# Kernel tuning notes

Hardware: AMD Instinct MI355X
Metric: run time of the kernel (lower is better)

## Reference

```python
import jax, jax.numpy as jnp
import numpy as np

B, S, D, H = 2, 2048, 2048, 16
HD = D // H  # 128
ROPE_BASE = 10000.0


def _rope_tables(seq_len, head_dim, dtype=jnp.float32):
    inv_freq = 1.0 / (ROPE_BASE ** (jnp.arange(0, head_dim, 2, dtype=jnp.float32) / head_dim))
    t = jnp.arange(seq_len, dtype=jnp.float32)
    freqs = jnp.outer(t, inv_freq)  # [S, HD/2]
    # broadcast shape [1, S, 1, HD/2]
    return jnp.cos(freqs)[None, :, None, :].astype(dtype), jnp.sin(freqs)[None, :, None, :].astype(dtype)


def _apply_rope(x, cos, sin):
    # x: [B, S, H, HD]; interleaved split, output concatenated by halves (matches torch code)
    x1 = x[..., ::2]
    x2 = x[..., 1::2]
    return jnp.concatenate([x1 * cos - x2 * sin, x1 * sin + x2 * cos], axis=-1)


def setup_inputs() -> dict:
    key = jax.random.key(0)
    ks = jax.random.split(key, 9)
    xavier = lambda k: jax.random.uniform(k, (D, D), jnp.float32, -1.0, 1.0) * np.sqrt(6.0 / (D + D))
    return {
        "x": jax.random.normal(ks[0], (B, S, D), jnp.float32),
        "attention_mask": jnp.ones((B, S), jnp.int32),
        "wq": xavier(ks[1]), "bq": jnp.zeros((D,), jnp.float32),
        "wk": xavier(ks[2]), "bk": jnp.zeros((D,), jnp.float32),
        "wv": xavier(ks[3]), "bv": jnp.zeros((D,), jnp.float32),
        "wo": xavier(ks[4]), "bo": jnp.zeros((D,), jnp.float32),
    }


def reference(x, attention_mask, wq, bq, wk, bk, wv, bv, wo, bo):
    b, s, _ = x.shape
    scale = HD ** -0.5
    q = (x @ wq + bq).reshape(b, s, H, HD)
    k = (x @ wk + bk).reshape(b, s, H, HD)
    v = (x @ wv + bv).reshape(b, s, H, HD)
    cos, sin = _rope_tables(s, HD, x.dtype)
    q = _apply_rope(q, cos, sin)
    k = _apply_rope(k, cos, sin)
    # [B, H, S, S]
    scores = jnp.einsum('bqhd,bkhd->bhqk', q, k) * scale
    mask = attention_mask[:, None, None, :]  # 2D mask -> [B,1,1,S]
    scores = jnp.where(mask == 0, jnp.asarray(-1e9, scores.dtype), scores)
    attn = jax.nn.softmax(scores, axis=-1)
    out = jnp.einsum('bhqk,bkhd->bqhd', attn, v).reshape(b, s, D)
    return out @ wo + bo
```

## Files before the change

### kernel.cpp

```cpp
#include <hip/hip_runtime.h>

#define Bc 2
#define Sc 2048
#define Dc 2048
#define Hc 16
#define HDc 128
#define Mc 4096

typedef __bf16 bf16_t;
typedef __bf16 bf16x4 __attribute__((ext_vector_type(4)));
typedef __bf16 bf16x8 __attribute__((ext_vector_type(8)));
typedef float f32x4 __attribute__((ext_vector_type(4)));
typedef float f32x16 __attribute__((ext_vector_type(16)));

__device__ __forceinline__ f32x4 mfma16(bf16x8 a, bf16x8 b, f32x4 c) {
  return __builtin_amdgcn_mfma_f32_16x16x32_bf16(a, b, c, 0, 0, 0);
}
__device__ __forceinline__ f32x16 mfma32(bf16x8 a, bf16x8 b, f32x16 c) {
  return __builtin_amdgcn_mfma_f32_32x32x16_bf16(a, b, c, 0, 0, 0);
}

typedef const unsigned __attribute__((address_space(1))) gu32_t;
typedef unsigned __attribute__((address_space(3))) lu32_t;

__device__ __forceinline__ void gload_lds16(const void* g, void* l) {
  gu32_t* gp = (gu32_t*)(unsigned long long)g;
  lu32_t* lp = (lu32_t*)(unsigned)(unsigned long long)l;
  __builtin_amdgcn_global_load_lds(gp, lp, 16, 0, 0);
}

__device__ __forceinline__ unsigned cvtpk(float lo, float hi_) {
  unsigned r;
  asm("v_cvt_pk_bf16_f32 %0, %1, %2" : "=v"(r) : "v"(lo), "v"(hi_));
  return r;
}
__device__ __forceinline__ void plswap(unsigned& a, unsigned& b) {
  asm volatile("v_permlane32_swap_b32 %0, %1" : "+v"(a), "+v"(b));
}

__global__ void cvt_bf16_kernel(const float* __restrict__ in, bf16_t* __restrict__ out, int n4) {
  int i = blockIdx.x * blockDim.x + threadIdx.x;
  if (i < n4) {
    float4 v = ((const float4*)in)[i];
    bf16x4 o;
    o[0] = (bf16_t)v.x; o[1] = (bf16_t)v.y; o[2] = (bf16_t)v.z; o[3] = (bf16_t)v.w;
    ((bf16x4*)out)[i] = o;
  }
}

__global__ void transpose_cvt_kernel(const float* __restrict__ w, bf16_t* __restrict__ wt) {
  __shared__ float tile[32][33];
  const int tx = threadIdx.x, ty = threadIdx.y;
  const int n0 = blockIdx.x * 32, k0 = blockIdx.y * 32;
#pragma unroll
  for (int i = 0; i < 32; i += 8)
    tile[ty + i][tx] = w[(size_t)(k0 + ty + i) * Dc + n0 + tx];
  __syncthreads();
#pragma unroll
  for (int i = 0; i < 32; i += 8)
    wt[(size_t)(n0 + ty + i) * Dc + k0 + tx] = (bf16_t)tile[tx][ty + i];
}

template <int MODE>
__global__ __launch_bounds__(256) void gemm_bt_kernel(
    const bf16_t* __restrict__ A, const bf16_t* __restrict__ Bt,
    const float* __restrict__ bias, void* __restrict__ outp, const int K) {
  __shared__ __align__(16) bf16_t sA[128 * 64];
  __shared__ __align__(16) bf16_t sB[128 * 64];
  const int w = threadIdx.x >> 6, lane = threadIdx.x & 63;
  const int l15 = lane & 15, g = lane >> 4;
  const int m0 = blockIdx.y * 128, n0 = blockIdx.x * 128;

  f32x4 acc[4][4] = {};

  for (int k0 = 0; k0 < K; k0 += 64) {
#pragma unroll
    for (int p = 0; p < 4; ++p) {
      int s_ = (p * 4 + w) * 64 + lane;
      int row = s_ >> 3, ch = s_ & 7;
      int sch = (ch ^ (row & 7)) * 8;
      gload_lds16(A + (size_t)(m0 + row) * K + k0 + sch,
                  (char*)sA + (size_t)((p * 4 + w) * 64) * 16);
      gload_lds16(Bt + (size_t)(n0 + row) * K + k0 + sch,
                  (char*)sB + (size_t)((p * 4 + w) * 64) * 16);
    }
    asm volatile("s_waitcnt vmcnt(0)" ::: "memory");
    __syncthreads();

    const int wm = (w >> 1) * 64, wn = (w & 1) * 64;
#pragma unroll
    for (int ks = 0; ks < 2; ++ks) {
      bf16x8 af[4], bfr[4];
#pragma unroll
      for (int i = 0; i < 4; ++i) {
        int ra = wm + i * 16 + l15;
        int ca = ((ks * 4 + g) ^ (ra & 7)) * 16;
        af[i] = *(const bf16x8*)((const char*)sA + ra * 128 + ca);
        int rb = wn + i * 16 + l15;
        int cb = ((ks * 4 + g) ^ (rb & 7)) * 16;
        bfr[i] = *(const bf16x8*)((const char*)sB + rb * 128 + cb);
      }
#pragma unroll
      for (int mi = 0; mi < 4; ++mi)
#pragma unroll
        for (int ni = 0; ni < 4; ++ni)
          acc[mi][ni] = mfma16(af[mi], bfr[ni], acc[mi][ni]);
    }
    __syncthreads();
  }

  const int wm = (w >> 1) * 64, wn = (w & 1) * 64;
#pragma unroll
  for (int mi = 0; mi < 4; ++mi) {
#pragma unroll
    for (int ni = 0; ni < 4; ++ni) {
      int ncol = n0 + wn + ni * 16 + l15;
      float bv = bias[ncol];
#pragma unroll
      for (int r = 0; r < 4; ++r) {
        int mrow = m0 + wm + mi * 16 + g * 4 + r;
        float v = acc[mi][ni][r] + bv;
        if (MODE == 2) {
          ((float*)outp)[(size_t)mrow * Dc + ncol] = v;
        } else {
          int b = mrow >> 11, sq = mrow & (Sc - 1);
          int h = ncol >> 7, hd = ncol & (HDc - 1);
          if (MODE == 0)
            ((bf16_t*)outp)[(((size_t)(b * Hc + h) * Sc + sq) * HDc) + hd] = (bf16_t)v;
          else
            ((bf16_t*)outp)[(((size_t)(b * Hc + h) * HDc + hd) * Sc) + sq] = (bf16_t)v;
        }
      }
    }
  }
}

__global__ __launch_bounds__(256) void rope_kernel(bf16_t* __restrict__ qk) {
  const int w = threadIdx.x >> 6, lane = threadIdx.x & 63;
  const long row = (long)blockIdx.x * 4 + w;
  const int s = (int)(row & (Sc - 1));
  bf16_t* p = qk + row * HDc;
  float x1 = (float)p[2 * lane];
  float x2 = (float)p[2 * lane + 1];
  float freq = expf(-(float)lane * (9.210340371976184f / 64.0f));
  float ang = (float)s * freq;
  float sn, cs;
  sincosf(ang, &sn, &cs);
  __syncthreads();
  p[lane] = (bf16_t)(x1 * cs - x2 * sn);
  p[lane + 64] = (bf16_t)(x1 * sn + x2 * cs);
}

__global__ __launch_bounds__(256, 2) void attn_kernel(
    const bf16_t* __restrict__ Q, const bf16_t* __restrict__ Kr,
    const bf16_t* __restrict__ Vt, const int* __restrict__ mask,
    bf16_t* __restrict__ AO) {
  __shared__ __align__(16) bf16_t sK[2][64 * 128];
  __shared__ __align__(16) bf16_t sV[2][128 * 64];
  __shared__ float mbias[Sc];
  __shared__ float bcast[4][32];
  const int tid = threadIdx.x;
  const int w = tid >> 6, lane = tid & 63;
  const int l31 = lane & 31, hi = lane >> 5;
  const int wbase = w * 64;

  const int bid = blockIdx.x;
  const int L = ((bid & 7) << 6) + (bid >> 3);
  const int qc = L & 15, h = (L >> 4) & 15, b = L >> 8;

  const int* mb = mask + b * Sc;
#pragma unroll
  for (int i = 0; i < Sc / 256; ++i)
    mbias[i * 256 + tid] = mb[i * 256 + tid] ? 0.f : -1e9f;

  const int q0 = qc * 128 + w * 32;
  const bf16_t* qb = Q + ((size_t)(b * Hc + h) * Sc + q0) * HDc;
  const bf16_t* kb = Kr + ((size_t)(b * Hc + h) * Sc) * HDc;
  const bf16_t* vb = Vt + ((size_t)(b * Hc + h) * HDc) * Sc;

  bf16x8 qf[8];
  {
    const bf16_t* qr = qb + (size_t)l31 * HDc + hi * 8;
#pragma unroll
    for (int kk = 0; kk < 8; ++kk) qf[kk] = *(const bf16x8*)(qr + kk * 16);
  }

#define STAGE_KV(sKb, sVb, kv0_)                                            \
  {                                                                         \
    _Pragma("unroll") for (int p = 0; p < 4; ++p) {                         \
      int s_ = p * 256 + tid;                                               \
      int rk = s_ >> 4, ck = s_ & 15;                                       \
      gload_lds16(kb + (size_t)((kv0_) + rk) * HDc + ((ck ^ (rk & 7)) * 8), \
                  (char*)(sKb) + (size_t)(p * 256 + wbase) * 16);           \
      int rv = s_ >> 3, cv = s_ & 7;                                        \
      gload_lds16(vb + (size_t)rv * Sc + (kv0_) + ((cv ^ (rv & 7)) * 8),    \
                  (char*)(sVb) + (size_t)(p * 256 + wbase) * 16);           \
    }                                                                       \
  }

  bf16_t* sKc = &sK[0][0];
  bf16_t* sKn = &sK[1][0];
  bf16_t* sVc = &sV[0][0];
  bf16_t* sVn = &sV[1][0];

  STAGE_KV(sKc, sVc, 0);
  asm volatile("s_waitcnt vmcnt(0)" ::: "memory");
  __syncthreads();

  f32x16 acc[4];
#pragma unroll
  for (int d = 0; d < 4; ++d) acc[d] = 0.f;
  float mrun = -3.0e38f, lrun = 0.f;
  const float scale = 0.08838834764831845f;

  for (int kv0 = 0; kv0 < Sc; kv0 += 64) {
    if (kv0 + 64 < Sc) STAGE_KV(sKn, sVn, kv0 + 64);

    f32x16 s0 = 0.f, s1 = 0.f;
    {
      const char* kbase = (const char*)sKc;
      const int swz = ((l31 & 7) ^ hi) * 16;
#pragma unroll
      for (int kk = 0; kk < 8; ++kk) {
        bf16x8 k0f = *(const bf16x8*)(kbase + l31 * 256 + (((2 * kk + hi) ^ (l31 & 7)) * 16));
        bf16x8 k1f = *(const bf16x8*)(kbase + (32 + l31) * 256 + (((2 * kk + hi) ^ (l31 & 7)) * 16));
        s0 = mfma32(k0f, qf[kk], s0);
        s1 = mfma32(k1f, qf[kk], s1);
      }
      (void)swz;
    }
    float v[32];
    {
      const float* mp = mbias + kv0 + 4 * hi;
#pragma unroll
      for (int g4 = 0; g4 < 4; ++g4) {
        f32x4 b0 = *(const f32x4*)(mp + 8 * g4);
        f32x4 b1 = *(const f32x4*)(mp + 32 + 8 * g4);
#pragma unroll
        for (int j = 0; j < 4; ++j) {
          v[g4 * 4 + j] = s0[g4 * 4 + j] * scale + b0[j];
          v[16 + g4 * 4 + j] = s1[g4 * 4 + j] * scale + b1[j];
        }
      }
    }
    float tm = v[0];
#pragma unroll
    for (int r = 1; r < 32; ++r) tm = fmaxf(tm, v[r]);
    tm = fmaxf(tm, __shfl_xor(tm, 32));
    if (__any(tm > mrun + 8.f)) {
      float mnew = fmaxf(mrun, tm);
      float al = __expf(mrun - mnew);
      mrun = mnew;
      lrun *= al;
      bcast[w][l31] = al;
      asm volatile("s_waitcnt lgkmcnt(0)" ::: "memory");
      __builtin_amdgcn_sched_barrier(0);
#pragma unroll
      for (int g4 = 0; g4 < 4; ++g4) {
        f32x4 alr = *(const f32x4*)(&bcast[w][8 * g4 + 4 * hi]);
#pragma unroll
        for (int dblk = 0; dblk < 4; ++dblk)
#pragma unroll
          for (int j = 0; j < 4; ++j) acc[dblk][g4 * 4 + j] *= alr[j];
      }
    }
    float ts = 0.f;
#pragma unroll
    for (int r = 0; r < 32; ++r) {
      v[r] = __expf(v[r] - mrun);
      ts += v[r];
    }
    ts += __shfl_xor(ts, 32);
    lrun += ts;
    unsigned pk[4][4];
#pragma unroll
    for (int ks = 0; ks < 4; ++ks) {
      unsigned a1 = cvtpk(v[ks * 8 + 0], v[ks * 8 + 1]);
      unsigned b1 = cvtpk(v[ks * 8 + 4], v[ks * 8 + 5]);
      unsigned a2 = cvtpk(v[ks * 8 + 2], v[ks * 8 + 3]);
      unsigned b2 = cvtpk(v[ks * 8 + 6], v[ks * 8 + 7]);
      plswap(a1, b1);
      plswap(a2, b2);
      pk[ks][0] = a1; pk[ks][1] = a2; pk[ks][2] = b1; pk[ks][3] = b2;
    }
    {
      const char* vbase = (const char*)sVc;
#pragma unroll
      for (int ks = 0; ks < 4; ++ks) {
        bf16x8 pa = *(const bf16x8*)&pk[ks][0];
#pragma unroll
        for (int dblk = 0; dblk < 4; ++dblk) {
          int d = dblk * 32 + l31;
          bf16x8 vf = *(const bf16x8*)(vbase + d * 128 + (((2 * ks + hi) ^ (d & 7)) * 16));
          acc[dblk] = mfma32(pa, vf, acc[dblk]);
        }
      }
    }
    asm volatile("s_waitcnt vmcnt(0)" ::: "memory");
    __syncthreads();
    bf16_t* t1 = sKc; sKc = sKn; sKn = t1;
    bf16_t* t2 = sVc; sVc = sVn; sVn = t2;
  }

  float inv = 1.f / lrun;
  bcast[w][l31] = inv;
  asm volatile("s_waitcnt lgkmcnt(0)" ::: "memory");
  __builtin_amdgcn_sched_barrier(0);
  bf16_t* ob = AO + ((size_t)b * Sc + q0) * Dc + h * HDc;
#pragma unroll
  for (int g4 = 0; g4 < 4; ++g4) {
    f32x4 ir = *(const f32x4*)(&bcast[w][8 * g4 + 4 * hi]);
#pragma unroll
    for (int j = 0; j < 4; ++j) {
      int q = 8 * g4 + 4 * hi + j;
#pragma unroll
      for (int dblk = 0; dblk < 4; ++dblk)
        ob[(size_t)q * Dc + dblk * 32 + l31] = (bf16_t)(acc[dblk][g4 * 4 + j] * ir[j]);
    }
  }
}

#define MB(x) ((size_t)(x) << 20)

extern "C" void kernel_launch(void* const* d_in, const int* in_sizes, int n_in,
                              void* d_out, int out_size, void* d_ws, size_t ws_size,
                              hipStream_t stream) {
  const float* x = (const float*)d_in[0];
  const int* mask = (const int*)d_in[1];
  const float* wq = (const float*)d_in[2];
  const float* bq = (const float*)d_in[3];
  const float* wk = (const float*)d_in[4];
  const float* bk = (const float*)d_in[5];
  const float* wv = (const float*)d_in[6];
  const float* bv = (const float*)d_in[7];
  const float* wo = (const float*)d_in[8];
  const float* bo = (const float*)d_in[9];
  float* out = (float*)d_out;

  char* ws = (char*)d_ws;
  bf16_t* xb  = (bf16_t*)(ws + MB(0));
  bf16_t* wqT = (bf16_t*)(ws + MB(16));
  bf16_t* wkT = (bf16_t*)(ws + MB(24));
  bf16_t* wvT = (bf16_t*)(ws + MB(32));
  bf16_t* woT = (bf16_t*)(ws + MB(40));
  bf16_t* qbuf = (bf16_t*)(ws + MB(48));
  bf16_t* kbuf = (bf16_t*)(ws + MB(64));
  bf16_t* vtb  = (bf16_t*)(ws + MB(80));
  bf16_t* ao   = (bf16_t*)(ws + MB(96));

  cvt_bf16_kernel<<<8192, 256, 0, stream>>>(x, xb, (Mc * Dc) / 4);

  dim3 tg(64, 64), tb(32, 8);
  transpose_cvt_kernel<<<tg, tb, 0, stream>>>(wq, wqT);
  transpose_cvt_kernel<<<tg, tb, 0, stream>>>(wk, wkT);
  transpose_cvt_kernel<<<tg, tb, 0, stream>>>(wv, wvT);
  transpose_cvt_kernel<<<tg, tb, 0, stream>>>(wo, woT);

  dim3 gg(Dc / 128, Mc / 128);
  gemm_bt_kernel<0><<<gg, 256, 0, stream>>>(xb, wqT, bq, qbuf, Dc);
  gemm_bt_kernel<0><<<gg, 256, 0, stream>>>(xb, wkT, bk, kbuf, Dc);
  gemm_bt_kernel<1><<<gg, 256, 0, stream>>>(xb, wvT, bv, vtb, Dc);

  rope_kernel<<<(2 * Bc * Hc * Sc) / 4, 256, 0, stream>>>(qbuf);

  attn_kernel<<<Bc * Hc * (Sc / 128), 256, 0, stream>>>(qbuf, kbuf, vtb, mask, ao);

  gemm_bt_kernel<2><<<gg, 256, 0, stream>>>(ao, woT, bo, out, Dc);
}
```

Before: 310.8 us.

## Fuse QKV GEMMs into one 256x256-tile pipelined GEMM with block swizzle

Replaces the 128x128 single-buffered GEMM with a 512-thread 256x256-tile kernel that uses a 4-slot LDS ring, prefetching three K-steps ahead with partial vmcnt waits. The Q, K and V projections are merged into a single launch over a concatenated transposed weight, and a block-index swizzle groups tiles for L2 reuse. s_setprio hints are added around the MFMA sections in both the GEMM and the attention kernel. The aim is to raise MFMA utilisation and hide global-load latency, at the cost of higher register and LDS pressure and fewer blocks for the output projection (128 blocks).

```diff
diff --git a/kernel.cpp b/kernel.cpp
--- a/kernel.cpp
+++ b/kernel.cpp
@@ -61,74 +61,104 @@
     wt[(size_t)(n0 + ty + i) * Dc + k0 + tx] = (bf16_t)tile[tx][ty + i];
 }
 
-template <int MODE>
-__global__ __launch_bounds__(256) void gemm_bt_kernel(
+template <int MODE, int NT>
+__global__ __launch_bounds__(512, 2) void gemm8_kernel(
     const bf16_t* __restrict__ A, const bf16_t* __restrict__ Bt,
-    const float* __restrict__ bias, void* __restrict__ outp, const int K) {
-  __shared__ __align__(16) bf16_t sA[128 * 64];
-  __shared__ __align__(16) bf16_t sB[128 * 64];
-  const int w = threadIdx.x >> 6, lane = threadIdx.x & 63;
+    const float* __restrict__ bias0, const float* __restrict__ bias1,
+    const float* __restrict__ bias2,
+    void* __restrict__ out0, void* __restrict__ out1, void* __restrict__ out2) {
+  __shared__ __align__(16) bf16_t sA[4][256 * 32];
+  __shared__ __align__(16) bf16_t sB[4][256 * 32];
+  const int tid = threadIdx.x;
+  const int lane = tid & 63, wid = tid >> 6;
   const int l15 = lane & 15, g = lane >> 4;
-  const int m0 = blockIdx.y * 128, n0 = blockIdx.x * 128;
-
-  f32x4 acc[4][4] = {};
-
-  for (int k0 = 0; k0 < K; k0 += 64) {
-#pragma unroll
-    for (int p = 0; p < 4; ++p) {
-      int s_ = (p * 4 + w) * 64 + lane;
-      int row = s_ >> 3, ch = s_ & 7;
-      int sch = (ch ^ (row & 7)) * 8;
-      gload_lds16(A + (size_t)(m0 + row) * K + k0 + sch,
-                  (char*)sA + (size_t)((p * 4 + w) * 64) * 16);
-      gload_lds16(Bt + (size_t)(n0 + row) * K + k0 + sch,
-                  (char*)sB + (size_t)((p * 4 + w) * 64) * 16);
-    }
-    asm volatile("s_waitcnt vmcnt(0)" ::: "memory");
-    __syncthreads();
-
-    const int wm = (w >> 1) * 64, wn = (w & 1) * 64;
-#pragma unroll
-    for (int ks = 0; ks < 2; ++ks) {
-      bf16x8 af[4], bfr[4];
-#pragma unroll
-      for (int i = 0; i < 4; ++i) {
-        int ra = wm + i * 16 + l15;
-        int ca = ((ks * 4 + g) ^ (ra & 7)) * 16;
-        af[i] = *(const bf16x8*)((const char*)sA + ra * 128 + ca);
-        int rb = wn + i * 16 + l15;
-        int cb = ((ks * 4 + g) ^ (rb & 7)) * 16;
-        bfr[i] = *(const bf16x8*)((const char*)sB + rb * 128 + cb);
-      }
-#pragma unroll
-      for (int mi = 0; mi < 4; ++mi)
-#pragma unroll
-        for (int ni = 0; ni < 4; ++ni)
-          acc[mi][ni] = mfma16(af[mi], bfr[ni], acc[mi][ni]);
-    }
-    __syncthreads();
-  }
-
-  const int wm = (w >> 1) * 64, wn = (w & 1) * 64;
-#pragma unroll
-  for (int mi = 0; mi < 4; ++mi) {
+  const int wrow = wid >> 2, wcol = wid & 3;
+
+  const int cpx = (NT * 16) / 8;
+  const int swz = ((int)blockIdx.x & 7) * cpx + ((int)blockIdx.x >> 3);
+  const int m0 = (swz / NT) * 256, n0 = (swz % NT) * 256;
+
+  const bf16_t* Ab = A + (size_t)m0 * 2048;
+  const bf16_t* Bb = Bt + (size_t)n0 * 2048;
+
+#define G8_STAGE(kt)                                                            \
+  {                                                                             \
+    const int sl_ = (kt) & 3;                                                   \
+    _Pragma("unroll") for (int i_ = 0; i_ < 2; ++i_) {                          \
+      int s_ = i_ * 512 + tid;                                                  \
+      int r_ = s_ >> 2, c_ = s_ & 3;                                            \
+      int sc_ = (kt) * 32 + ((c_ ^ (r_ & 3)) * 8);                              \
+      gload_lds16(Ab + (size_t)r_ * 2048 + sc_, (char*)&sA[sl_][0] + s_ * 16);  \
+      gload_lds16(Bb + (size_t)r_ * 2048 + sc_, (char*)&sB[sl_][0] + s_ * 16);  \
+    }                                                                           \
+  }
+
+  f32x4 acc[8][4] = {};
+
+  G8_STAGE(0);
+  G8_STAGE(1);
+  G8_STAGE(2);
+
+#define G8_BODY(t, DOSTG, VMSTR)                                              \
+  {                                                                           \
+    asm volatile("s_waitcnt vmcnt(" VMSTR ")" ::: "memory");                  \
+    __builtin_amdgcn_s_barrier();                                             \
+    __builtin_amdgcn_sched_barrier(0);                                        \
+    const int sl = (t) & 3;                                                   \
+    const char* pA = (const char*)&sA[sl][0];                                 \
+    const char* pB = (const char*)&sB[sl][0];                                 \
+    bf16x8 bfrag[4], afrag[8];                                                \
+    _Pragma("unroll") for (int ni = 0; ni < 4; ++ni) {                        \
+      int rb = wcol * 64 + ni * 16 + l15;                                     \
+      bfrag[ni] = *(const bf16x8*)(pB + rb * 64 + ((g ^ (rb & 3)) * 16));     \
+    }                                                                         \
+    _Pragma("unroll") for (int mi = 0; mi < 8; ++mi) {                        \
+      int ra = wrow * 128 + mi * 16 + l15;                                    \
+      afrag[mi] = *(const bf16x8*)(pA + ra * 64 + ((g ^ (ra & 3)) * 16));     \
+    }                                                                         \
+    if (DOSTG) G8_STAGE((t) + 3);                                             \
+    __builtin_amdgcn_s_setprio(1);                                            \
+    _Pragma("unroll") for (int mi = 0; mi < 8; ++mi)                          \
+      _Pragma("unroll") for (int ni = 0; ni < 4; ++ni)                        \
+          acc[mi][ni] = mfma16(afrag[mi], bfrag[ni], acc[mi][ni]);            \
+    __builtin_amdgcn_s_setprio(0);                                            \
+  }
+
+  for (int t = 0; t < 61; ++t) G8_BODY(t, 1, "8");
+  G8_BODY(61, 0, "8");
+  G8_BODY(62, 0, "4");
+  G8_BODY(63, 0, "0");
+
+#undef G8_BODY
+#undef G8_STAGE
+
+#pragma unroll
+  for (int mi = 0; mi < 8; ++mi) {
 #pragma unroll
     for (int ni = 0; ni < 4; ++ni) {
-      int ncol = n0 + wn + ni * 16 + l15;
-      float bv = bias[ncol];
-#pragma unroll
-      for (int r = 0; r < 4; ++r) {
-        int mrow = m0 + wm + mi * 16 + g * 4 + r;
-        float v = acc[mi][ni][r] + bv;
-        if (MODE == 2) {
-          ((float*)outp)[(size_t)mrow * Dc + ncol] = v;
-        } else {
-          int b = mrow >> 11, sq = mrow & (Sc - 1);
-          int h = ncol >> 7, hd = ncol & (HDc - 1);
-          if (MODE == 0)
-            ((bf16_t*)outp)[(((size_t)(b * Hc + h) * Sc + sq) * HDc) + hd] = (bf16_t)v;
+      const int ncol = n0 + wcol * 64 + ni * 16 + l15;
+      if (MODE == 2) {
+        const float bv = bias0[ncol];
+#pragma unroll
+        for (int r = 0; r < 4; ++r) {
+          const int mrow = m0 + wrow * 128 + mi * 16 + g * 4 + r;
+          ((float*)out0)[(size_t)mrow * 2048 + ncol] = acc[mi][ni][r] + bv;
+        }
+      } else {
+        const int proj = ncol >> 11, nloc = ncol & 2047;
+        const float* bp = proj == 0 ? bias0 : (proj == 1 ? bias1 : bias2);
+        bf16_t* op = (bf16_t*)(proj == 0 ? out0 : (proj == 1 ? out1 : out2));
+        const float bv = bp[nloc];
+        const int h = nloc >> 7, hd = nloc & 127;
+#pragma unroll
+        for (int r = 0; r < 4; ++r) {
+          const int mrow = m0 + wrow * 128 + mi * 16 + g * 4 + r;
+          const int b = mrow >> 11, sq = mrow & 2047;
+          const float v = acc[mi][ni][r] + bv;
+          if (proj < 2)
+            op[(((size_t)(b * Hc + h) * Sc + sq) * HDc) + hd] = (bf16_t)v;
           else
-            ((bf16_t*)outp)[(((size_t)(b * Hc + h) * HDc + hd) * Sc) + sq] = (bf16_t)v;
+            op[(((size_t)(b * Hc + h) * HDc + hd) * Sc) + sq] = (bf16_t)v;
         }
       }
     }
@@ -219,7 +249,7 @@
     f32x16 s0 = 0.f, s1 = 0.f;
     {
       const char* kbase = (const char*)sKc;
-      const int swz = ((l31 & 7) ^ hi) * 16;
+      __builtin_amdgcn_s_setprio(1);
 #pragma unroll
       for (int kk = 0; kk < 8; ++kk) {
         bf16x8 k0f = *(const bf16x8*)(kbase + l31 * 256 + (((2 * kk + hi) ^ (l31 & 7)) * 16));
@@ -227,7 +257,7 @@
         s0 = mfma32(k0f, qf[kk], s0);
         s1 = mfma32(k1f, qf[kk], s1);
       }
-      (void)swz;
+      __builtin_amdgcn_s_setprio(0);
     }
     float v[32];
     {
@@ -285,6 +315,7 @@
     }
     {
       const char* vbase = (const char*)sVc;
+      __builtin_amdgcn_s_setprio(1);
 #pragma unroll
       for (int ks = 0; ks < 4; ++ks) {
         bf16x8 pa = *(const bf16x8*)&pk[ks][0];
@@ -295,6 +326,7 @@
           acc[dblk] = mfma32(pa, vf, acc[dblk]);
         }
       }
+      __builtin_amdgcn_s_setprio(0);
     }
     asm volatile("s_waitcnt vmcnt(0)" ::: "memory");
     __syncthreads();
@@ -338,32 +370,27 @@
   float* out = (float*)d_out;
 
   char* ws = (char*)d_ws;
-  bf16_t* xb  = (bf16_t*)(ws + MB(0));
-  bf16_t* wqT = (bf16_t*)(ws + MB(16));
-  bf16_t* wkT = (bf16_t*)(ws + MB(24));
-  bf16_t* wvT = (bf16_t*)(ws + MB(32));
-  bf16_t* woT = (bf16_t*)(ws + MB(40));
-  bf16_t* qbuf = (bf16_t*)(ws + MB(48));
-  bf16_t* kbuf = (bf16_t*)(ws + MB(64));
-  bf16_t* vtb  = (bf16_t*)(ws + MB(80));
-  bf16_t* ao   = (bf16_t*)(ws + MB(96));
+  bf16_t* xb     = (bf16_t*)(ws + MB(0));
+  bf16_t* wqkvT  = (bf16_t*)(ws + MB(16));
+  bf16_t* woT    = (bf16_t*)(ws + MB(40));
+  bf16_t* qbuf   = (bf16_t*)(ws + MB(48));
+  bf16_t* kbuf   = (bf16_t*)(ws + MB(64));
+  bf16_t* vtb    = (bf16_t*)(ws + MB(80));
+  bf16_t* ao     = (bf16_t*)(ws + MB(96));
 
   cvt_bf16_kernel<<<8192, 256, 0, stream>>>(x, xb, (Mc * Dc) / 4);
 
   dim3 tg(64, 64), tb(32, 8);
-  transpose_cvt_kernel<<<tg, tb, 0, stream>>>(wq, wqT);
-  transpose_cvt_kernel<<<tg, tb, 0, stream>>>(wk, wkT);
-  transpose_cvt_kernel<<<tg, tb, 0, stream>>>(wv, wvT);
+  transpose_cvt_kernel<<<tg, tb, 0, stream>>>(wq, wqkvT);
+  transpose_cvt_kernel<<<tg, tb, 0, stream>>>(wk, wqkvT + (size_t)Dc * Dc);
+  transpose_cvt_kernel<<<tg, tb, 0, stream>>>(wv, wqkvT + 2 * (size_t)Dc * Dc);
   transpose_cvt_kernel<<<tg, tb, 0, stream>>>(wo, woT);
 
-  dim3 gg(Dc / 128, Mc / 128);
-  gemm_bt_kernel<0><<<gg, 256, 0, stream>>>(xb, wqT, bq, qbuf, Dc);
-  gemm_bt_kernel<0><<<gg, 256, 0, stream>>>(xb, wkT, bk, kbuf, Dc);
-  gemm_bt_kernel<1><<<gg, 256, 0, stream>>>(xb, wvT, bv, vtb, Dc);
+  gemm8_kernel<0, 24><<<384, 512, 0, stream>>>(xb, wqkvT, bq, bk, bv, qbuf, kbuf, vtb);
 
   rope_kernel<<<(2 * Bc * Hc * Sc) / 4, 256, 0, stream>>>(qbuf);
 
   attn_kernel<<<Bc * Hc * (Sc / 128), 256, 0, stream>>>(qbuf, kbuf, vtb, mask, ao);
 
-  gemm_bt_kernel<2><<<gg, 256, 0, stream>>>(ao, woT, bo, out, Dc);
-}
+  gemm8_kernel<2, 8><<<128, 512, 0, stream>>>(ao, woT, bo, bo, bo, out, out, out);
+}
```

New measurement: 333.0 us. 7.2% more time.
